# Optimization experiments

Measured on AMD Instinct MI355X. Metric: run time of the kernel, lower is better.

The kernel has to match this reference:

```python
import jax, jax.numpy as jnp
import numpy as np

NEG_SLOPE = 0.2  # PyG GATConv default


def _gat_conv(x, src, dst, W, a_src, a_dst, b, heads, out_ch, concat, n):
    """PyG-style GATConv. src/dst already include self-loops. a_*: (heads, out_ch)."""
    h = (x @ W).reshape(n, heads, out_ch)                      # (n, H, C)
    alpha_s = jnp.einsum('nhc,hc->nh', h, a_src)               # (n, H)
    alpha_d = jnp.einsum('nhc,hc->nh', h, a_dst)
    e = jax.nn.leaky_relu(alpha_s[src] + alpha_d[dst], NEG_SLOPE)   # (Etot, H)
    # segment softmax over destination nodes (numerically stable)
    m = jax.ops.segment_max(e, dst, num_segments=n)            # (n, H)
    w = jnp.exp(e - m[dst])
    denom = jax.ops.segment_sum(w, dst, num_segments=n)
    att = w / (denom[dst] + 1e-16)                             # (Etot, H)
    out = jax.ops.segment_sum(h[src] * att[:, :, None], dst, num_segments=n)  # (n, H, C)
    out = out.reshape(n, heads * out_ch) if concat else out.mean(axis=1)
    return out + b


def setup_inputs() -> dict:
    key = jax.random.key(0)
    ks = jax.random.split(key, 16)
    N, E, D, Hc, H, M = 50000, 400000, 256, 128, 4, 256

    def glorot(k, shape):
        fan_in, fan_out = shape[0], int(np.prod(shape[1:]))
        std = float(np.sqrt(2.0 / (fan_in + fan_out)))
        return jax.random.normal(k, shape, dtype=jnp.float32) * std

    return {
        'x': jax.random.normal(ks[0], (N, D), dtype=jnp.float32),
        'edge_index': jax.random.randint(ks[1], (2, E), 0, N, dtype=jnp.int64),
        # encoder layer 1: D -> (H, Hc), concat
        'W1': glorot(ks[2], (D, H * Hc)),
        'a_src1': glorot(ks[3], (H, Hc)),
        'a_dst1': glorot(ks[4], (H, Hc)),
        'b1': jnp.zeros((H * Hc,), dtype=jnp.float32),
        'prelu_a': jnp.full((1,), 0.25, dtype=jnp.float32),
        # encoder layer 2: H*Hc -> M, 1 head, no concat
        'W2': glorot(ks[5], (H * Hc, M)),
        'a_src2': glorot(ks[6], (1, M)),
        'a_dst2': glorot(ks[7], (1, M)),
        'b2': jnp.zeros((M,), dtype=jnp.float32),
        # decoder: M -> D, 1 head, no concat
        'Wd': glorot(ks[8], (M, D)),
        'a_srcd': glorot(ks[9], (1, D)),
        'a_dstd': glorot(ks[10], (1, D)),
        'bd': jnp.zeros((D,), dtype=jnp.float32),
    }


def reference(x, edge_index, W1, a_src1, a_dst1, b1, prelu_a,
              W2, a_src2, a_dst2, b2, Wd, a_srcd, a_dstd, bd):
    n = x.shape[0]
    loop = jnp.arange(n, dtype=edge_index.dtype)
    src = jnp.concatenate([edge_index[0], loop])  # self-loops (PyG default)
    dst = jnp.concatenate([edge_index[1], loop])

    # --- encoder (eval mode: no masking, dropout off) ---
    h = _gat_conv(x, src, dst, W1, a_src1, a_dst1, b1, heads=4, out_ch=128, concat=True, n=n)
    h = jnp.where(h >= 0, h, prelu_a * h)  # PReLU
    z = _gat_conv(h, src, dst, W2, a_src2, a_dst2, b2, heads=1, out_ch=256, concat=False, n=n)

    # --- decoder (single GAT, no activation) ---
    x_hat = _gat_conv(z, src, dst, Wd, a_srcd, a_dstd, bd, heads=1, out_ch=256, concat=False, n=n)
    return (z, x_hat)
```

## Files before the change

### kernel.cpp

```cpp
#include <hip/hip_runtime.h>
#include <hip/hip_bf16.h>
#include <cstdint>

#define NEG_SLOPE 0.2f

typedef _Float16 f16x8 __attribute__((ext_vector_type(8)));
typedef float f32x4 __attribute__((ext_vector_type(4)));

union H2 { uint32_t u; _Float16 f[2]; };
union H8 { uint4 u4; _Float16 f[8]; };

__global__ void k_init_counts(int* __restrict__ counts, int n) {
  int i = blockIdx.x * blockDim.x + threadIdx.x;
  if (i < n) counts[i] = 1;
}

__global__ void k_hist(const int* __restrict__ dst, int* __restrict__ counts, int e) {
  int i = blockIdx.x * blockDim.x + threadIdx.x;
  if (i < e) atomicAdd(&counts[dst[i]], 1);
}

__global__ void k_scan1(const int* __restrict__ counts, int* __restrict__ pref,
                        int* __restrict__ bsum, int n) {
  __shared__ int sh[256];
  int tid = threadIdx.x;
  int i = blockIdx.x * 256 + tid;
  int v = (i < n) ? counts[i] : 0;
  sh[tid] = v;
  __syncthreads();
  for (int off = 1; off < 256; off <<= 1) {
    int t = (tid >= off) ? sh[tid - off] : 0;
    __syncthreads();
    sh[tid] += t;
    __syncthreads();
  }
  if (i < n) pref[i] = sh[tid];
  if (tid == 255) bsum[blockIdx.x] = sh[255];
}

__global__ void k_scan2(int* __restrict__ bsum, int nb) {
  __shared__ int sh[256];
  int tid = threadIdx.x;
  int v = (tid < nb) ? bsum[tid] : 0;
  sh[tid] = v;
  __syncthreads();
  for (int off = 1; off < 256; off <<= 1) {
    int t = (tid >= off) ? sh[tid - off] : 0;
    __syncthreads();
    sh[tid] += t;
    __syncthreads();
  }
  if (tid < nb) bsum[tid] = sh[tid];
}

__global__ void k_scan3(const int* __restrict__ pref, const int* __restrict__ bsum,
                        int* __restrict__ rowptr, int n) {
  int i = blockIdx.x * blockDim.x + threadIdx.x;
  if (i < n) rowptr[i + 1] = pref[i] + (blockIdx.x ? bsum[blockIdx.x - 1] : 0);
  if (i == 0) rowptr[0] = 0;
}

__global__ void k_init_csr(const int* __restrict__ rowptr, int* __restrict__ cursor,
                           int* __restrict__ csr_src, int n) {
  int i = blockIdx.x * blockDim.x + threadIdx.x;
  if (i < n) { int r = rowptr[i]; csr_src[r] = i; cursor[i] = r + 1; }
}

__global__ void k_fill(const int* __restrict__ src, const int* __restrict__ dst,
                       int* __restrict__ cursor, int* __restrict__ csr_src, int e) {
  int i = blockIdx.x * blockDim.x + threadIdx.x;
  if (i < e) { int p = atomicAdd(&cursor[dst[i]], 1); csr_src[p] = src[i]; }
}

__global__ void k_w2h(const float* __restrict__ W, _Float16* __restrict__ Wt, int K, int N) {
  int i = blockIdx.x * blockDim.x + threadIdx.x;
  if (i < K * N) {
    int k = i / N, n = i - k * N;
    Wt[(size_t)n * K + k] = (_Float16)W[i];
  }
}

template <bool A_F32>
__global__ __launch_bounds__(512) void k_gemm_f16(
    const void* __restrict__ Av, const _Float16* __restrict__ Bt,
    _Float16* __restrict__ C, int M, int N, int K) {
  __shared__ _Float16 As[256 * 72];
  __shared__ _Float16 Bs[128 * 72];
  const int tid  = threadIdx.x;
  const int lane = tid & 63;
  const int wid  = tid >> 6;
  const int wm = wid >> 1;
  const int wn = wid & 1;
  const int row0 = blockIdx.y * 256, col0 = blockIdx.x * 128;
  const int l15 = lane & 15, l16 = lane >> 4;
  const int srow = tid >> 3;
  const int skc  = (tid & 7) * 8;

  f32x4 acc[4][4] = {};

  for (int k0 = 0; k0 < K; k0 += 64) {
#pragma unroll
    for (int p = 0; p < 4; ++p) {
      int r = p * 64 + srow;
      int gr = row0 + r; if (gr > M - 1) gr = M - 1;
      _Float16 tmp[8];
      if constexpr (A_F32) {
        const float* src = (const float*)Av + (size_t)gr * K + k0 + skc;
        float4 v0 = ((const float4*)src)[0];
        float4 v1 = ((const float4*)src)[1];
        tmp[0] = (_Float16)v0.x; tmp[1] = (_Float16)v0.y;
        tmp[2] = (_Float16)v0.z; tmp[3] = (_Float16)v0.w;
        tmp[4] = (_Float16)v1.x; tmp[5] = (_Float16)v1.y;
        tmp[6] = (_Float16)v1.z; tmp[7] = (_Float16)v1.w;
      } else {
        const _Float16* src = (const _Float16*)Av + (size_t)gr * K + k0 + skc;
        *(uint4*)tmp = *(const uint4*)src;
      }
      *(uint4*)&As[r * 72 + skc] = *(uint4*)tmp;
    }
#pragma unroll
    for (int p = 0; p < 2; ++p) {
      int nr_ = p * 64 + srow;
      const _Float16* src = Bt + (size_t)(col0 + nr_) * K + k0 + skc;
      *(uint4*)&Bs[nr_ * 72 + skc] = *(const uint4*)src;
    }
    __syncthreads();
#pragma unroll
    for (int ks = 0; ks < 2; ++ks) {
      f16x8 bfrag[4];
#pragma unroll
      for (int nr = 0; nr < 4; ++nr)
        bfrag[nr] = *(const f16x8*)&Bs[(wn * 64 + nr * 16 + l15) * 72 + ks * 32 + l16 * 8];
#pragma unroll
      for (int mr = 0; mr < 4; ++mr) {
        f16x8 afrag = *(const f16x8*)&As[(wm * 64 + mr * 16 + l15) * 72 + ks * 32 + l16 * 8];
#pragma unroll
        for (int nr = 0; nr < 4; ++nr)
          acc[mr][nr] = __builtin_amdgcn_mfma_f32_16x16x32_f16(afrag, bfrag[nr], acc[mr][nr], 0, 0, 0);
      }
    }
    __syncthreads();
  }
#pragma unroll
  for (int mr = 0; mr < 4; ++mr) {
#pragma unroll
    for (int j = 0; j < 4; ++j) {
      int rg = row0 + wm * 64 + mr * 16 + l16 * 4 + j;
      if (rg < M) {
#pragma unroll
        for (int nr = 0; nr < 4; ++nr) {
          int cg = col0 + wn * 64 + nr * 16 + l15;
          C[(size_t)rg * N + cg] = (_Float16)acc[mr][nr][j];
        }
      }
    }
  }
}

template <int H, int CH>
__global__ void k_alpha(const _Float16* __restrict__ h, const float* __restrict__ a_src,
                        const float* __restrict__ a_dst, float* __restrict__ as,
                        float* __restrict__ ad, int total) {
  int wid = (blockIdx.x * blockDim.x + threadIdx.x) >> 6;
  int lane = threadIdx.x & 63;
  if (wid >= total) return;
  int head = wid % H;
  const _Float16* hp = h + (size_t)wid * CH;
  const float* asp = a_src + head * CH;
  const float* adp = a_dst + head * CH;
  float s1 = 0.f, s2 = 0.f;
  for (int c = lane * 2; c < CH; c += 128) {
    H2 v; v.u = *(const uint32_t*)&hp[c];
    float v0 = (float)v.f[0], v1 = (float)v.f[1];
    s1 += v0 * asp[c] + v1 * asp[c + 1];
    s2 += v0 * adp[c] + v1 * adp[c + 1];
  }
#pragma unroll
  for (int off = 32; off; off >>= 1) {
    s1 += __shfl_down(s1, off);
    s2 += __shfl_down(s2, off);
  }
  if (lane == 0) { as[wid] = s1; ad[wid] = s2; }
}

template <int W>
__device__ __forceinline__ float grp_sum(float v) {
#pragma unroll
  for (int o = W / 2; o; o >>= 1) v += __shfl_xor(v, o);
  return v;
}

template <int CT, int H, int ACT, int WF, int WH>
__global__ __launch_bounds__(256) void k_agg(
    const _Float16* __restrict__ h, const float* __restrict__ as,
    const float* __restrict__ ad, const int* __restrict__ rowptr,
    const int* __restrict__ csr, const float* __restrict__ bias,
    const float* __restrict__ prelu_a, float* __restrict__ outf,
    _Float16* __restrict__ outh, int n) {
  constexpr int CH  = CT / H;
  constexpr int TPN = CT / 8;
  constexpr int NSW = 64 / TPN;
  constexpr int G   = CH / 8;

  int lane = threadIdx.x & 63;
  int wib  = threadIdx.x >> 6;
  int slot0  = (blockIdx.x * (256 >> 6) + wib) * NSW + ((NSW == 2) ? (lane >> 5) : 0);
  int stride = gridDim.x * (256 >> 6) * NSW;
  int nt   = lane & (TPN - 1);
  int c0   = nt * 8;
  int head = c0 / CH;
  int gl   = lane & (G - 1);
  int srcbase = (lane / G) * G;

  float a_prelu = ACT ? prelu_a[0] : 0.f;
  float4 bv0 = *(const float4*)&bias[c0];
  float4 bv1 = *(const float4*)&bias[c0 + 4];

  for (int node = slot0; node < n; node += stride) {
    int beg = rowptr[node];
    int cnt = rowptr[node + 1] - beg;
    float adv = ad[node * H + head];
    float denom = 0.f;
    float acc[8] = {};
    for (int b = 0; b < cnt; b += G) {
      int i = b + gl;
      float w = 0.f; int s = 0;
      if (i < cnt) {
        s = csr[beg + i];
        float v = as[s * H + head] + adv;
        v = (v >= 0.f) ? v : NEG_SLOPE * v;
        w = __expf(v);
      }
      denom += grp_sum<G>(w);
      int nedge = cnt - b; if (nedge > G) nedge = G;
      int kk = 0;
      for (; kk + 4 <= nedge; kk += 4) {
        int sj[4]; float wj[4]; H8 uj[4];
#pragma unroll
        for (int j = 0; j < 4; ++j) {
          sj[j] = __shfl(s, srcbase + kk + j);
          wj[j] = __shfl(w, srcbase + kk + j);
        }
#pragma unroll
        for (int j = 0; j < 4; ++j)
          uj[j].u4 = *(const uint4*)&h[(size_t)sj[j] * CT + c0];
#pragma unroll
        for (int j = 0; j < 4; ++j) {
#pragma unroll
          for (int q = 0; q < 8; ++q) acc[q] += wj[j] * (float)uj[j].f[q];
        }
      }
      {
        int rem = nedge - kk;
        int sj[3]; float wj[3]; H8 uj[3];
#pragma unroll
        for (int j = 0; j < 3; ++j) {
          if (j < rem) {
            sj[j] = __shfl(s, srcbase + kk + j);
            wj[j] = __shfl(w, srcbase + kk + j);
          }
        }
#pragma unroll
        for (int j = 0; j < 3; ++j)
          if (j < rem) uj[j].u4 = *(const uint4*)&h[(size_t)sj[j] * CT + c0];
#pragma unroll
        for (int j = 0; j < 3; ++j) {
          if (j < rem) {
#pragma unroll
            for (int q = 0; q < 8; ++q) acc[q] += wj[j] * (float)uj[j].f[q];
          }
        }
      }
    }

    float inv = 1.f / (denom + 1e-16f);
    float o[8];
    o[0] = acc[0] * inv + bv0.x; o[1] = acc[1] * inv + bv0.y;
    o[2] = acc[2] * inv + bv0.z; o[3] = acc[3] * inv + bv0.w;
    o[4] = acc[4] * inv + bv1.x; o[5] = acc[5] * inv + bv1.y;
    o[6] = acc[6] * inv + bv1.z; o[7] = acc[7] * inv + bv1.w;
    if (ACT) {
#pragma unroll
      for (int q = 0; q < 8; ++q) o[q] = (o[q] >= 0.f) ? o[q] : a_prelu * o[q];
    }
    if (WF) {
      *(float4*)&outf[(size_t)node * CT + c0]     = make_float4(o[0], o[1], o[2], o[3]);
      *(float4*)&outf[(size_t)node * CT + c0 + 4] = make_float4(o[4], o[5], o[6], o[7]);
    }
    if (WH) {
      H8 p;
#pragma unroll
      for (int q = 0; q < 8; ++q) p.f[q] = (_Float16)o[q];
      *(uint4*)&outh[(size_t)node * CT + c0] = p.u4;
    }
  }
}

extern "C" void kernel_launch(void* const* d_in, const int* in_sizes, int n_in,
                              void* d_out, int out_size, void* d_ws, size_t ws_size,
                              hipStream_t stream) {
  const float* x      = (const float*)d_in[0];
  const int*   ei     = (const int*)d_in[1];
  const float* W1     = (const float*)d_in[2];
  const float* a_s1   = (const float*)d_in[3];
  const float* a_d1   = (const float*)d_in[4];
  const float* b1     = (const float*)d_in[5];
  const float* prelu  = (const float*)d_in[6];
  const float* W2     = (const float*)d_in[7];
  const float* a_s2   = (const float*)d_in[8];
  const float* a_d2   = (const float*)d_in[9];
  const float* b2     = (const float*)d_in[10];
  const float* Wd     = (const float*)d_in[11];
  const float* a_sd   = (const float*)d_in[12];
  const float* a_dd   = (const float*)d_in[13];
  const float* bd     = (const float*)d_in[14];

  const int N = in_sizes[0] / 256;
  const int E = in_sizes[1] / 2;
  const int* e_src = ei;
  const int* e_dst = ei + E;

  float* z    = (float*)d_out;
  float* xhat = z + (size_t)N * 256;

  _Float16* out1_h = (_Float16*)xhat;

  char* wp = (char*)d_ws;
  auto alloc = [&](size_t bytes) { char* p = wp; wp += (bytes + 15) & ~(size_t)15; return p; };
  _Float16* h_h  = (_Float16*)alloc((size_t)N * 512 * 2);
  float* alpS    = (float*)alloc((size_t)N * 4 * 4);
  float* alpD    = (float*)alloc((size_t)N * 4 * 4);
  int* rowptr    = (int*)alloc((size_t)(N + 1) * 4);
  int* csr       = (int*)alloc((size_t)(E + N) * 4);
  int* cursor    = (int*)alloc((size_t)N * 4);
  int* counts    = (int*)alloc((size_t)N * 4);
  int* pref      = (int*)alloc((size_t)N * 4);
  int* bsum      = (int*)alloc((size_t)256 * 4);
  _Float16* Wt1  = (_Float16*)alloc((size_t)512 * 256 * 2);
  _Float16* Wt2  = (_Float16*)alloc((size_t)256 * 512 * 2);
  _Float16* Wtd  = (_Float16*)alloc((size_t)256 * 256 * 2);

  const int B = 256;
  const int gN = (N + B - 1) / B;
  const int gE = (E + B - 1) / B;
  const int AGG_GRID = 2048;

  k_init_counts<<<gN, B, 0, stream>>>(counts, N);
  k_hist<<<gE, B, 0, stream>>>(e_dst, counts, E);
  k_scan1<<<gN, B, 0, stream>>>(counts, pref, bsum, N);
  k_scan2<<<1, B, 0, stream>>>(bsum, gN);
  k_scan3<<<gN, B, 0, stream>>>(pref, bsum, rowptr, N);
  k_init_csr<<<gN, B, 0, stream>>>(rowptr, cursor, csr, N);
  k_fill<<<gE, B, 0, stream>>>(e_src, e_dst, cursor, csr, E);

  k_w2h<<<(256 * 512 + B - 1) / B, B, 0, stream>>>(W1, Wt1, 256, 512);
  k_w2h<<<(512 * 256 + B - 1) / B, B, 0, stream>>>(W2, Wt2, 512, 256);
  k_w2h<<<(256 * 256 + B - 1) / B, B, 0, stream>>>(Wd, Wtd, 256, 256);

  const int gy = (N + 255) / 256;

  {
    dim3 grid(512 / 128, gy);
    k_gemm_f16<true><<<grid, 512, 0, stream>>>(x, Wt1, h_h, N, 512, 256);
    int tot = N * 4;
    k_alpha<4, 128><<<(tot * 64 + B - 1) / B, B, 0, stream>>>(h_h, a_s1, a_d1, alpS, alpD, tot);
    k_agg<512, 4, 1, 0, 1><<<AGG_GRID, B, 0, stream>>>(
        h_h, alpS, alpD, rowptr, csr, b1, prelu, nullptr, out1_h, N);
  }

  {
    dim3 grid(256 / 128, gy);
    k_gemm_f16<false><<<grid, 512, 0, stream>>>(out1_h, Wt2, h_h, N, 256, 512);
    k_alpha<1, 256><<<(N * 64 + B - 1) / B, B, 0, stream>>>(h_h, a_s2, a_d2, alpS, alpD, N);
    k_agg<256, 1, 0, 1, 0><<<AGG_GRID, B, 0, stream>>>(
        h_h, alpS, alpD, rowptr, csr, b2, prelu, z, nullptr, N);
  }

  {
    dim3 grid(256 / 128, gy);
    k_gemm_f16<true><<<grid, 512, 0, stream>>>(z, Wtd, h_h, N, 256, 256);
    k_alpha<1, 256><<<(N * 64 + B - 1) / B, B, 0, stream>>>(h_h, a_sd, a_dd, alpS, alpD, N);
    k_agg<256, 1, 0, 1, 0><<<AGG_GRID, B, 0, stream>>>(
        h_h, alpS, alpD, rowptr, csr, bd, prelu, xhat, nullptr, N);
  }
}
```

Measured before the change: 524.9 us.

## Fuse attention logit computation into GEMM epilogue

Computes the per-node source and destination attention scores inside the f16 MFMA GEMM epilogue, using the fp16-rounded accumulators, a 16-lane shuffle reduction and shared memory. This replaces the separate k_alpha kernels that re-read h from global memory. When one head's width spans two column blocks (the single-head layers), partial sums are combined with atomicAdd, which needs a zeroing kernel first. It trades one read pass over h per layer for a longer epilogue, atomics and a different floating-point summation order.

```diff
diff --git a/kernel.cpp b/kernel.cpp
--- a/kernel.cpp
+++ b/kernel.cpp
@@ -72,6 +72,11 @@
   if (i < e) { int p = atomicAdd(&cursor[dst[i]], 1); csr_src[p] = src[i]; }
 }
 
+__global__ void k_zero2(float* __restrict__ a, float* __restrict__ b, int n) {
+  int i = blockIdx.x * blockDim.x + threadIdx.x;
+  if (i < n) { a[i] = 0.f; b[i] = 0.f; }
+}
+
 __global__ void k_w2h(const float* __restrict__ W, _Float16* __restrict__ Wt, int K, int N) {
   int i = blockIdx.x * blockDim.x + threadIdx.x;
   if (i < K * N) {
@@ -80,10 +85,12 @@
   }
 }
 
-template <bool A_F32>
+template <bool A_F32, int H, bool ALPHA_ATOMIC>
 __global__ __launch_bounds__(512) void k_gemm_f16(
     const void* __restrict__ Av, const _Float16* __restrict__ Bt,
-    _Float16* __restrict__ C, int M, int N, int K) {
+    _Float16* __restrict__ C, const float* __restrict__ aS,
+    const float* __restrict__ aD, float* __restrict__ alpS,
+    float* __restrict__ alpD, int M, int N, int K) {
   __shared__ _Float16 As[256 * 72];
   __shared__ _Float16 Bs[128 * 72];
   const int tid  = threadIdx.x;
@@ -141,6 +148,7 @@
     }
     __syncthreads();
   }
+
 #pragma unroll
   for (int mr = 0; mr < 4; ++mr) {
 #pragma unroll
@@ -155,32 +163,54 @@
       }
     }
   }
-}
-
-template <int H, int CH>
-__global__ void k_alpha(const _Float16* __restrict__ h, const float* __restrict__ a_src,
-                        const float* __restrict__ a_dst, float* __restrict__ as,
-                        float* __restrict__ ad, int total) {
-  int wid = (blockIdx.x * blockDim.x + threadIdx.x) >> 6;
-  int lane = threadIdx.x & 63;
-  if (wid >= total) return;
-  int head = wid % H;
-  const _Float16* hp = h + (size_t)wid * CH;
-  const float* asp = a_src + head * CH;
-  const float* adp = a_dst + head * CH;
-  float s1 = 0.f, s2 = 0.f;
-  for (int c = lane * 2; c < CH; c += 128) {
-    H2 v; v.u = *(const uint32_t*)&hp[c];
-    float v0 = (float)v.f[0], v1 = (float)v.f[1];
-    s1 += v0 * asp[c] + v1 * asp[c + 1];
-    s2 += v0 * adp[c] + v1 * adp[c + 1];
-  }
-#pragma unroll
-  for (int off = 32; off; off >>= 1) {
-    s1 += __shfl_down(s1, off);
-    s2 += __shfl_down(s2, off);
-  }
-  if (lane == 0) { as[wid] = s1; ad[wid] = s2; }
+
+  float avs[4], avd[4];
+#pragma unroll
+  for (int nr = 0; nr < 4; ++nr) {
+    int cg = col0 + wn * 64 + nr * 16 + l15;
+    avs[nr] = aS[cg];
+    avd[nr] = aD[cg];
+  }
+  float* alp = (float*)As;
+#pragma unroll
+  for (int mr = 0; mr < 4; ++mr) {
+#pragma unroll
+    for (int j = 0; j < 4; ++j) {
+      float hs = 0.f, hd = 0.f;
+#pragma unroll
+      for (int nr = 0; nr < 4; ++nr) {
+        float v = (float)(_Float16)acc[mr][nr][j];
+        hs += v * avs[nr];
+        hd += v * avd[nr];
+      }
+#pragma unroll
+      for (int o = 1; o < 16; o <<= 1) {
+        hs += __shfl_xor(hs, o);
+        hd += __shfl_xor(hd, o);
+      }
+      if (l15 == 0) {
+        int r = wm * 64 + mr * 16 + l16 * 4 + j;
+        alp[(wn * 256 + r) * 2 + 0] = hs;
+        alp[(wn * 256 + r) * 2 + 1] = hd;
+      }
+    }
+  }
+  __syncthreads();
+  if (tid < 256) {
+    int rg = row0 + tid;
+    if (rg < M) {
+      float s_ = alp[tid * 2 + 0] + alp[(256 + tid) * 2 + 0];
+      float d_ = alp[tid * 2 + 1] + alp[(256 + tid) * 2 + 1];
+      int head = (int)((long)col0 * H / N);
+      if (ALPHA_ATOMIC) {
+        atomicAdd(&alpS[rg * H + head], s_);
+        atomicAdd(&alpD[rg * H + head], d_);
+      } else {
+        alpS[rg * H + head] = s_;
+        alpD[rg * H + head] = d_;
+      }
+    }
+  }
 }
 
 template <int W>
@@ -361,25 +391,26 @@
 
   {
     dim3 grid(512 / 128, gy);
-    k_gemm_f16<true><<<grid, 512, 0, stream>>>(x, Wt1, h_h, N, 512, 256);
-    int tot = N * 4;
-    k_alpha<4, 128><<<(tot * 64 + B - 1) / B, B, 0, stream>>>(h_h, a_s1, a_d1, alpS, alpD, tot);
+    k_gemm_f16<true, 4, false><<<grid, 512, 0, stream>>>(
+        x, Wt1, h_h, a_s1, a_d1, alpS, alpD, N, 512, 256);
     k_agg<512, 4, 1, 0, 1><<<AGG_GRID, B, 0, stream>>>(
         h_h, alpS, alpD, rowptr, csr, b1, prelu, nullptr, out1_h, N);
   }
 
   {
+    k_zero2<<<gN, B, 0, stream>>>(alpS, alpD, N);
     dim3 grid(256 / 128, gy);
-    k_gemm_f16<false><<<grid, 512, 0, stream>>>(out1_h, Wt2, h_h, N, 256, 512);
-    k_alpha<1, 256><<<(N * 64 + B - 1) / B, B, 0, stream>>>(h_h, a_s2, a_d2, alpS, alpD, N);
+    k_gemm_f16<false, 1, true><<<grid, 512, 0, stream>>>(
+        out1_h, Wt2, h_h, a_s2, a_d2, alpS, alpD, N, 256, 512);
     k_agg<256, 1, 0, 1, 0><<<AGG_GRID, B, 0, stream>>>(
         h_h, alpS, alpD, rowptr, csr, b2, prelu, z, nullptr, N);
   }
 
   {
+    k_zero2<<<gN, B, 0, stream>>>(alpS, alpD, N);
     dim3 grid(256 / 128, gy);
-    k_gemm_f16<true><<<grid, 512, 0, stream>>>(z, Wtd, h_h, N, 256, 256);
-    k_alpha<1, 256><<<(N * 64 + B - 1) / B, B, 0, stream>>>(h_h, a_sd, a_dd, alpS, alpD, N);
+    k_gemm_f16<true, 1, true><<<grid, 512, 0, stream>>>(
+        z, Wtd, h_h, a_sd, a_dd, alpS, alpD, N, 256, 256);
     k_agg<256, 1, 0, 1, 0><<<AGG_GRID, B, 0, stream>>>(
         h_h, alpS, alpD, rowptr, csr, bd, prelu, xhat, nullptr, N);
   }
```

Result: faster. 495.5 us (-5.6%).
